# Kernel tuning notes

Hardware: AMD Instinct MI355X
Metric: run time of the kernel (lower is better)

## Reference

```python
import jax, jax.numpy as jnp
import numpy as np

N = 500000
V = 50000
GF = 64
OC = 256

def _lin(key, din, dout):
    k1, k2 = jax.random.split(key)
    w = jax.random.normal(k1, (din, dout), dtype=jnp.float32) * 0.02
    b = jax.random.normal(k2, (dout,), dtype=jnp.float32) * 0.02
    return w, b

def setup_inputs() -> dict:
    key = jax.random.key(0)
    ks = jax.random.split(key, 12)
    inp_feat = jax.random.normal(ks[0], (N, 6), dtype=jnp.float32)
    vox2point_idx = jax.random.randint(ks[1], (N,), 0, V, dtype=jnp.int32)
    w1x, b1x = _lin(ks[2], 3, GF)
    w2x, b2x = _lin(ks[3], GF, OC // 8)
    w1r, b1r = _lin(ks[4], 3, GF)
    w2r, b2r = _lin(ks[5], GF, OC // 8)
    wax, bax = _lin(ks[6], OC // 4, OC // 8)
    war, bar = _lin(ks[7], OC // 4, OC // 8)
    wv1, bv1 = _lin(ks[8], OC // 2, OC // 2)
    w3, b3 = _lin(ks[9], OC, OC)
    w4, b4 = _lin(ks[10], OC, OC)
    wv2, bv2 = _lin(ks[11], OC, OC)
    return dict(inp_feat=inp_feat, vox2point_idx=vox2point_idx, num_vox=V,
                w1x=w1x, b1x=b1x, w2x=w2x, b2x=b2x,
                w1r=w1r, b1r=b1r, w2r=w2r, b2r=b2r,
                wax=wax, bax=bax, war=war, bar=bar,
                wv1=wv1, bv1=bv1, w3=w3, b3=b3, w4=w4, b4=b4,
                wv2=wv2, bv2=bv2)

def reference(inp_feat, vox2point_idx, num_vox,
              w1x, b1x, w2x, b2x, w1r, b1r, w2r, b2r,
              wax, bax, war, bar, wv1, bv1, w3, b3, w4, b4, wv2, bv2):
    relu = jax.nn.relu
    xyz = inp_feat[:, :3]
    rgb = inp_feat[:, 3:]
    fx = relu(relu(xyz @ w1x + b1x) @ w2x + b2x)   # [N, 32]
    fr = relu(relu(rgb @ w1r + b1r) @ w2r + b2r)   # [N, 32]
    comb = jnp.concatenate([fx, fr], axis=-1)       # [N, 64]
    pf2 = jnp.concatenate([
        fx, fx * jax.nn.sigmoid(comb @ wax + bax),
        fr, fr * jax.nn.sigmoid(comb @ war + bar)], axis=-1)  # [N, 128]
    # scatter-max to voxels; torch_scatter fills empty segments with 0 and
    # pf2 >= 0 elementwise, so clamp -inf (jax empty fill) to 0 for parity.
    vox = jax.ops.segment_max(pf2, vox2point_idx, num_segments=num_vox)
    vox = jnp.maximum(vox, 0.0)                     # [V, 128]
    vox = relu(vox @ wv1 + bv1)
    pg = vox[vox2point_idx]                          # gather back [N, 128]
    pf3 = jnp.concatenate([pg, pf2], axis=-1)        # [N, 256]
    pf5 = relu(relu(pf3 @ w3 + b3) @ w4 + b4)        # [N, 256]
    vox2 = jax.ops.segment_max(pf5, vox2point_idx, num_segments=num_vox)
    vox2 = jnp.maximum(vox2, 0.0)
    return relu(vox2 @ wv2 + bv2)                    # [V, 256]
```

## Files before the change

### kernel.cpp

```cpp
#include <hip/hip_runtime.h>

#define NPTS 500000
#define NVOX 50000
#define NBLK 196

typedef unsigned short u16;
typedef unsigned int u32;
typedef __attribute__((ext_vector_type(8))) short short8;
typedef __attribute__((ext_vector_type(4))) float floatx4;
typedef __attribute__((ext_vector_type(4))) unsigned int uintx4;
typedef __attribute__((ext_vector_type(2))) unsigned int uintx2;

__device__ __forceinline__ u16 f2bf(float f) {
    u32 u = __float_as_uint(f);
    u = u + 0x7fffu + ((u >> 16) & 1u);
    return (u16)(u >> 16);
}

__global__ void k_wtransform(const float* __restrict__ W, u16* __restrict__ Wf, int K, int N) {
    int t = blockIdx.x * 256 + threadIdx.x;
    if (t >= K * N) return;
    int k = t / N, n = t - k * N;
    int kk = k >> 5, q = (k >> 3) & 3, j = k & 7;
    Wf[((size_t)((kk * 4 + q) * N + n) << 3) + j] = f2bf(W[t]);
}

__global__ void k_wcat(const float* __restrict__ w2x, const float* __restrict__ w2r, u16* __restrict__ wcatf) {
    int t = blockIdx.x * 256 + threadIdx.x;
    if (t >= 128 * 64) return;
    int k = t >> 6, n = t & 63;
    float v;
    if (k < 64) v = (n < 32) ? w2x[k * 32 + n] : 0.f;
    else        v = (n >= 32) ? w2r[(k - 64) * 32 + (n - 32)] : 0.f;
    int kk = k >> 5, q = (k >> 3) & 3, j = k & 7;
    wcatf[((size_t)((kk * 4 + q) * 64 + n) << 3) + j] = f2bf(v);
}

__global__ void k_watt(const float* __restrict__ wax, const float* __restrict__ war, u16* __restrict__ wattf) {
    int t = blockIdx.x * 256 + threadIdx.x;
    if (t >= 64 * 64) return;
    int k = t >> 6, n = t & 63;
    float v = (n < 32) ? wax[k * 32 + n] : war[k * 32 + (n - 32)];
    int kk = k >> 5, q = (k >> 3) & 3, j = k & 7;
    wattf[((size_t)((kk * 4 + q) * 64 + n) << 3) + j] = f2bf(v);
}

__global__ void k_hist(const int* __restrict__ idx, int* __restrict__ hcnt) {
    int i = blockIdx.x * 256 + threadIdx.x;
    if (i < NPTS) atomicAdd(&hcnt[idx[i]], 1);
}

__global__ __launch_bounds__(256) void k_scan1(const int* __restrict__ hcnt, int* __restrict__ bsum) {
    __shared__ int wsum[4];
    int t = threadIdx.x;
    int i = blockIdx.x * 256 + t;
    int c = (i < NVOX) ? hcnt[i] : 0;
    #pragma unroll
    for (int d = 32; d >= 1; d >>= 1) c += __shfl_xor(c, d, 64);
    if ((t & 63) == 0) wsum[t >> 6] = c;
    __syncthreads();
    if (t == 0) bsum[blockIdx.x] = wsum[0] + wsum[1] + wsum[2] + wsum[3];
}

__global__ __launch_bounds__(256) void k_scan2(const int* __restrict__ bsum, int* __restrict__ boff) {
    __shared__ int wsum[4];
    int t = threadIdx.x, lane = t & 63, w = t >> 6;
    int c = (t < NBLK) ? bsum[t] : 0;
    int v = c;
    #pragma unroll
    for (int d = 1; d < 64; d <<= 1) {
        int o = __shfl_up(v, d, 64);
        if (lane >= d) v += o;
    }
    if (lane == 63) wsum[w] = v;
    __syncthreads();
    int wo = 0;
    #pragma unroll
    for (int k = 0; k < 4; k++) if (k < w) wo += wsum[k];
    if (t < NBLK) boff[t] = wo + v - c;
}

__global__ __launch_bounds__(256) void k_scan3(const int* __restrict__ hcnt, const int* __restrict__ boff,
                                               int* __restrict__ cur) {
    __shared__ int wsum[4];
    int t = threadIdx.x, lane = t & 63, w = t >> 6;
    int i = blockIdx.x * 256 + t;
    int c = (i < NVOX) ? hcnt[i] : 0;
    int v = c;
    #pragma unroll
    for (int d = 1; d < 64; d <<= 1) {
        int o = __shfl_up(v, d, 64);
        if (lane >= d) v += o;
    }
    if (lane == 63) wsum[w] = v;
    __syncthreads();
    int wo = 0;
    #pragma unroll
    for (int k = 0; k < 4; k++) if (k < w) wo += wsum[k];
    if (i < NVOX) cur[i] = boff[blockIdx.x] + wo + v - c;
}

__global__ void k_scatter(const int* __restrict__ idx, int* __restrict__ cur,
                          int* __restrict__ sptid, int* __restrict__ svid) {
    int i = blockIdx.x * 256 + threadIdx.x;
    if (i < NPTS) {
        int v = idx[i];
        int pos = atomicAdd(&cur[v], 1);
        sptid[pos] = i;
        svid[pos] = v;
    }
}

__global__ __launch_bounds__(256) void k_pointfeat(
    const float* __restrict__ inp, const int* __restrict__ sptid, const int* __restrict__ svid,
    const float* __restrict__ w1x, const float* __restrict__ b1x,
    const float* __restrict__ w1r, const float* __restrict__ b1r,
    const u16* __restrict__ wcatf, const float* __restrict__ b2x, const float* __restrict__ b2r,
    const u16* __restrict__ wattf, const float* __restrict__ bax, const float* __restrict__ bar,
    u16* __restrict__ pf2s, float* __restrict__ voxmax)
{
    __shared__ u16 hbuf[64 * 136];
    __shared__ u16 cbuf[64 * 72];
    __shared__ float wl[512];
    __shared__ int lvid[64];
    int t = threadIdx.x;
    int i0 = blockIdx.x * 64;
    int mcnt = NPTS - i0; if (mcnt > 64) mcnt = 64;
    for (int s = t; s < 512; s += 256) {
        float v;
        if (s < 192)      v = w1x[s];
        else if (s < 256) v = b1x[s - 192];
        else if (s < 448) v = w1r[s - 256];
        else              v = b1r[s - 448];
        wl[s] = v;
    }
    if (t < 64) lvid[t] = (t < mcnt) ? svid[i0 + t] : -1;
    __syncthreads();
    {
        int m = t >> 2, c = t & 3;
        float x0 = 0, x1 = 0, x2 = 0, r0 = 0, r1 = 0, r2 = 0;
        if (m < mcnt) {
            const float* p = inp + (size_t)sptid[i0 + m] * 6;
            x0 = p[0]; x1 = p[1]; x2 = p[2]; r0 = p[3]; r1 = p[4]; r2 = p[5];
        }
        u16* hb = &hbuf[m * 136 + c * 16];
        #pragma unroll
        for (int jp = 0; jp < 8; jp++) {
            int c0 = c * 16 + 2 * jp, c1 = c0 + 1;
            float hx0 = fmaxf(wl[192 + c0] + x0 * wl[c0] + x1 * wl[64 + c0] + x2 * wl[128 + c0], 0.f);
            float hx1 = fmaxf(wl[192 + c1] + x0 * wl[c1] + x1 * wl[64 + c1] + x2 * wl[128 + c1], 0.f);
            float hr0 = fmaxf(wl[448 + c0] + r0 * wl[256 + c0] + r1 * wl[320 + c0] + r2 * wl[384 + c0], 0.f);
            float hr1 = fmaxf(wl[448 + c1] + r0 * wl[256 + c1] + r1 * wl[320 + c1] + r2 * wl[384 + c1], 0.f);
            *(u32*)(hb + 2 * jp)      = (u32)f2bf(hx0) | ((u32)f2bf(hx1) << 16);
            *(u32*)(hb + 64 + 2 * jp) = (u32)f2bf(hr0) | ((u32)f2bf(hr1) << 16);
        }
    }
    __syncthreads();
    int wave = t >> 6, l = t & 63, q = l >> 4, lm = l & 15;
    int n = wave * 16 + lm;
    floatx4 acc[4];
    #pragma unroll
    for (int a = 0; a < 4; a++) acc[a] = (floatx4){0.f, 0.f, 0.f, 0.f};
    #pragma unroll
    for (int kk = 0; kk < 4; kk++) {
        short8 bfrag = *(const short8*)&wcatf[(size_t)((kk * 4 + q) * 64 + n) << 3];
        #pragma unroll
        for (int tm = 0; tm < 4; tm++) {
            short8 afrag = *(const short8*)&hbuf[(tm * 16 + lm) * 136 + kk * 32 + q * 8];
            acc[tm] = __builtin_amdgcn_mfma_f32_16x16x32_bf16(afrag, bfrag, acc[tm], 0, 0, 0);
        }
    }
    float bv = (n < 32) ? b2x[n] : b2r[n - 32];
    float comb_keep[4][4];
    #pragma unroll
    for (int tm = 0; tm < 4; tm++)
        #pragma unroll
        for (int r = 0; r < 4; r++) {
            float v = fmaxf(acc[tm][r] + bv, 0.f);
            comb_keep[tm][r] = v;
            int m = tm * 16 + q * 4 + r;
            cbuf[m * 72 + n] = f2bf(v);
        }
    __syncthreads();
    floatx4 acc2[4];
    #pragma unroll
    for (int a = 0; a < 4; a++) acc2[a] = (floatx4){0.f, 0.f, 0.f, 0.f};
    #pragma unroll
    for (int kk = 0; kk < 2; kk++) {
        short8 bfrag = *(const short8*)&wattf[(size_t)((kk * 4 + q) * 64 + n) << 3];
        #pragma unroll
        for (int tm = 0; tm < 4; tm++) {
            short8 afrag = *(const short8*)&cbuf[(tm * 16 + lm) * 72 + kk * 32 + q * 8];
            acc2[tm] = __builtin_amdgcn_mfma_f32_16x16x32_bf16(afrag, bfrag, acc2[tm], 0, 0, 0);
        }
    }
    float bv2 = (n < 32) ? bax[n] : bar[n - 32];
    int pp = (n < 32) ? n : 32 + n;
    #pragma unroll
    for (int tm = 0; tm < 4; tm++)
        #pragma unroll
        for (int r = 0; r < 4; r++) {
            float att = acc2[tm][r] + bv2;
            float sg = 1.f / (1.f + __expf(-att));
            float plain = comb_keep[tm][r];
            float gated = plain * sg;
            int m = tm * 16 + q * 4 + r;
            hbuf[m * 136 + pp] = f2bf(plain);
            hbuf[m * 136 + pp + 32] = f2bf(gated);
        }
    __syncthreads();
    {
        int row = t >> 2, seg = t & 3;
        if (row < mcnt) {
            const u16* src = &hbuf[row * 136 + seg * 32];
            u16* dst = pf2s + (size_t)(i0 + row) * 128 + seg * 32;
            *(uintx4*)dst = *(const uintx4*)src;
            *(uintx4*)(dst + 8) = *(const uintx4*)(src + 8);
        }
    }
    {
        int c2 = t & 63;
        int h = t >> 6;
        int r0 = h * 16;
        int r1 = r0 + 16; if (r1 > mcnt) r1 = mcnt;
        u32 mlo = 0, mhi = 0;
        int pvid = -1;
        for (int r = r0; r < r1; r++) {
            int vid = lvid[r];
            if (vid != pvid) {
                if (pvid >= 0) {
                    int* addr = (int*)(voxmax + (size_t)pvid * 128 + 2 * c2);
                    if (mlo) atomicMax(addr, (int)(mlo << 16));
                    if (mhi) atomicMax(addr + 1, (int)(mhi << 16));
                }
                pvid = vid; mlo = 0; mhi = 0;
            }
            u32 u = *(const u32*)&hbuf[r * 136 + 2 * c2];
            u32 lo = u & 0xffffu, hi = u >> 16;
            mlo = lo > mlo ? lo : mlo;
            mhi = hi > mhi ? hi : mhi;
        }
        if (pvid >= 0) {
            int* addr = (int*)(voxmax + (size_t)pvid * 128 + 2 * c2);
            if (mlo) atomicMax(addr, (int)(mlo << 16));
            if (mhi) atomicMax(addr + 1, (int)(mhi << 16));
        }
    }
}

template<int K, int N, bool ABF16, bool OUT_BF16>
__global__ __launch_bounds__(256) void k_gemm_relu(
    const void* __restrict__ Ap, const u16* __restrict__ Wf,
    const float* __restrict__ bias, void* __restrict__ outp, int M)
{
    constexpr int STRIDE = K + 8;
    constexpr int TN = N / 64;
    constexpr int KSTEPS = K / 32;
    constexpr int CW = K / 4;
    __shared__ u16 lds[64 * STRIDE];
    int i0 = blockIdx.x * 64;
    int mcnt = M - i0; if (mcnt > 64) mcnt = 64;
    int t = threadIdx.x;
    {
        int row = t >> 2, cseg = t & 3;
        u16* dst = &lds[row * STRIDE + cseg * CW];
        if (row < mcnt) {
            if (ABF16) {
                const u16* src = (const u16*)Ap + (size_t)(i0 + row) * K + cseg * CW;
                #pragma unroll
                for (int c = 0; c < CW / 8; c++)
                    *(uintx4*)(dst + c * 8) = *(const uintx4*)(src + c * 8);
            } else {
                const float* src = (const float*)Ap + (size_t)(i0 + row) * K + cseg * CW;
                #pragma unroll
                for (int c = 0; c < CW / 8; c++) {
                    float4 v0 = *(const float4*)(src + c * 8);
                    float4 v1 = *(const float4*)(src + c * 8 + 4);
                    short8 rr;
                    rr[0] = f2bf(v0.x); rr[1] = f2bf(v0.y); rr[2] = f2bf(v0.z); rr[3] = f2bf(v0.w);
                    rr[4] = f2bf(v1.x); rr[5] = f2bf(v1.y); rr[6] = f2bf(v1.z); rr[7] = f2bf(v1.w);
                    *(short8*)(dst + c * 8) = rr;
                }
            }
        } else {
            short8 z = {0, 0, 0, 0, 0, 0, 0, 0};
            #pragma unroll
            for (int c = 0; c < CW / 8; c++) *(short8*)(dst + c * 8) = z;
        }
    }
    __syncthreads();
    int wave = t >> 6, l = t & 63;
    int q = l >> 4, lm = l & 15;
    int wn0 = wave * (N / 4);
    floatx4 acc[4][TN];
    #pragma unroll
    for (int a = 0; a < 4; a++)
        #pragma unroll
        for (int b = 0; b < TN; b++) acc[a][b] = (floatx4){0.f, 0.f, 0.f, 0.f};
    #pragma unroll
    for (int kk = 0; kk < KSTEPS; kk++) {
        short8 afrag[4], bfrag[TN];
        #pragma unroll
        for (int tm = 0; tm < 4; tm++)
            afrag[tm] = *(const short8*)&lds[(tm * 16 + lm) * STRIDE + kk * 32 + q * 8];
        #pragma unroll
        for (int tn = 0; tn < TN; tn++)
            bfrag[tn] = *(const short8*)&Wf[(size_t)((kk * 4 + q) * N + wn0 + tn * 16 + lm) * 8];
        #pragma unroll
        for (int tm = 0; tm < 4; tm++)
            #pragma unroll
            for (int tn = 0; tn < TN; tn++)
                acc[tm][tn] = __builtin_amdgcn_mfma_f32_16x16x32_bf16(afrag[tm], bfrag[tn], acc[tm][tn], 0, 0, 0);
    }
    #pragma unroll
    for (int tm = 0; tm < 4; tm++)
        #pragma unroll
        for (int tn = 0; tn < TN; tn++) {
            int n = wn0 + tn * 16 + lm;
            float bv = bias[n];
            #pragma unroll
            for (int r = 0; r < 4; r++) {
                int m = tm * 16 + q * 4 + r;
                if (m < mcnt) {
                    float v = fmaxf(acc[tm][tn][r] + bv, 0.f);
                    if (OUT_BF16) ((u16*)outp)[(size_t)(i0 + m) * N + n] = f2bf(v);
                    else          ((float*)outp)[(size_t)(i0 + m) * N + n] = v;
                }
            }
        }
}

__global__ __launch_bounds__(256) void k_pointmlp(
    const u16* __restrict__ voxf, const u16* __restrict__ pf2s, const int* __restrict__ svid,
    const u16* __restrict__ w3f, const float* __restrict__ b3,
    const u16* __restrict__ w4f, const float* __restrict__ b4,
    float* __restrict__ vox2)
{
    constexpr int STRIDE = 264;
    __shared__ u16 lds[64 * STRIDE];
    __shared__ int lvid[64];
    __shared__ float bl[512];
    int i0 = blockIdx.x * 64;
    int mcnt = NPTS - i0; if (mcnt > 64) mcnt = 64;
    int t = threadIdx.x;
    if (t < 64) lvid[t] = (t < mcnt) ? svid[i0 + t] : -1;
    for (int s = t; s < 512; s += 256) bl[s] = (s < 256) ? b3[s] : b4[s - 256];
    {
        int row = t >> 2, cseg = t & 3;
        u16* dst = &lds[row * STRIDE + cseg * 64];
        if (row < mcnt) {
            const u16* src;
            if (cseg < 2) src = voxf + (size_t)svid[i0 + row] * 128 + cseg * 64;
            else          src = pf2s + (size_t)(i0 + row) * 128 + (cseg - 2) * 64;
            #pragma unroll
            for (int c = 0; c < 8; c++)
                *(uintx4*)(dst + c * 8) = *(const uintx4*)(src + c * 8);
        } else {
            uintx4 z = {0, 0, 0, 0};
            #pragma unroll
            for (int c = 0; c < 8; c++) *(uintx4*)(dst + c * 8) = z;
        }
    }
    __syncthreads();
    int wave = t >> 6, l = t & 63;
    int q = l >> 4, lm = l & 15;
    int wm0 = wave * 64;
    floatx4 acc[4][4];
    #pragma unroll
    for (int a = 0; a < 4; a++)
        #pragma unroll
        for (int b = 0; b < 4; b++) acc[a][b] = (floatx4){0.f, 0.f, 0.f, 0.f};
    #pragma unroll
    for (int kk = 0; kk < 8; kk++) {
        short8 wfrag[4], bfrag[4];
        #pragma unroll
        for (int tm = 0; tm < 4; tm++)
            wfrag[tm] = *(const short8*)&w3f[(size_t)((kk * 4 + q) * 256 + wm0 + tm * 16 + lm) * 8];
        #pragma unroll
        for (int tn = 0; tn < 4; tn++)
            bfrag[tn] = *(const short8*)&lds[(tn * 16 + lm) * STRIDE + kk * 32 + q * 8];
        #pragma unroll
        for (int tm = 0; tm < 4; tm++)
            #pragma unroll
            for (int tn = 0; tn < 4; tn++)
                acc[tm][tn] = __builtin_amdgcn_mfma_f32_16x16x32_bf16(wfrag[tm], bfrag[tn], acc[tm][tn], 0, 0, 0);
    }
    __syncthreads();
    #pragma unroll
    for (int tm = 0; tm < 4; tm++) {
        float4 bq = *(const float4*)&bl[wm0 + tm * 16 + 4 * q];
        #pragma unroll
        for (int tn = 0; tn < 4; tn++) {
            u32 lo = (u32)f2bf(fmaxf(acc[tm][tn][0] + bq.x, 0.f)) | ((u32)f2bf(fmaxf(acc[tm][tn][1] + bq.y, 0.f)) << 16);
            u32 hi = (u32)f2bf(fmaxf(acc[tm][tn][2] + bq.z, 0.f)) | ((u32)f2bf(fmaxf(acc[tm][tn][3] + bq.w, 0.f)) << 16);
            *(uintx2*)&lds[(tn * 16 + lm) * STRIDE + wm0 + tm * 16 + 4 * q] = (uintx2){lo, hi};
        }
    }
    __syncthreads();
    floatx4 acc2[4][4];
    #pragma unroll
    for (int a = 0; a < 4; a++)
        #pragma unroll
        for (int b = 0; b < 4; b++) acc2[a][b] = (floatx4){0.f, 0.f, 0.f, 0.f};
    #pragma unroll
    for (int kk = 0; kk < 8; kk++) {
        short8 wfrag[4], bfrag[4];
        #pragma unroll
        for (int tm = 0; tm < 4; tm++)
            wfrag[tm] = *(const short8*)&w4f[(size_t)((kk * 4 + q) * 256 + wm0 + tm * 16 + lm) * 8];
        #pragma unroll
        for (int tn = 0; tn < 4; tn++)
            bfrag[tn] = *(const short8*)&lds[(tn * 16 + lm) * STRIDE + kk * 32 + q * 8];
        #pragma unroll
        for (int tm = 0; tm < 4; tm++)
            #pragma unroll
            for (int tn = 0; tn < 4; tn++)
                acc2[tm][tn] = __builtin_amdgcn_mfma_f32_16x16x32_bf16(wfrag[tm], bfrag[tn], acc2[tm][tn], 0, 0, 0);
    }
    __syncthreads();
    #pragma unroll
    for (int tm = 0; tm < 4; tm++) {
        float4 bq = *(const float4*)&bl[256 + wm0 + tm * 16 + 4 * q];
        #pragma unroll
        for (int tn = 0; tn < 4; tn++) {
            u32 lo = (u32)f2bf(fmaxf(acc2[tm][tn][0] + bq.x, 0.f)) | ((u32)f2bf(fmaxf(acc2[tm][tn][1] + bq.y, 0.f)) << 16);
            u32 hi = (u32)f2bf(fmaxf(acc2[tm][tn][2] + bq.z, 0.f)) | ((u32)f2bf(fmaxf(acc2[tm][tn][3] + bq.w, 0.f)) << 16);
            *(uintx2*)&lds[(tn * 16 + lm) * STRIDE + wm0 + tm * 16 + 4 * q] = (uintx2){lo, hi};
        }
    }
    __syncthreads();
    {
        int c2 = t & 127;
        int h = t >> 7;
        int r0 = h * 32;
        int r1 = r0 + 32; if (r1 > mcnt) r1 = mcnt;
        u32 mlo = 0, mhi = 0;
        int pvid = -1;
        for (int r = r0; r < r1; r++) {
            int vid = lvid[r];
            if (vid != pvid) {
                if (pvid >= 0) {
                    int* addr = (int*)(vox2 + (size_t)pvid * 256 + 2 * c2);
                    if (mlo) atomicMax(addr, (int)(mlo << 16));
                    if (mhi) atomicMax(addr + 1, (int)(mhi << 16));
                }
                pvid = vid; mlo = 0; mhi = 0;
            }
            u32 u = *(const u32*)&lds[r * STRIDE + 2 * c2];
            u32 lo = u & 0xffffu, hi = u >> 16;
            mlo = lo > mlo ? lo : mlo;
            mhi = hi > mhi ? hi : mhi;
        }
        if (pvid >= 0) {
            int* addr = (int*)(vox2 + (size_t)pvid * 256 + 2 * c2);
            if (mlo) atomicMax(addr, (int)(mlo << 16));
            if (mhi) atomicMax(addr + 1, (int)(mhi << 16));
        }
    }
}

extern "C" void kernel_launch(void* const* d_in, const int* in_sizes, int n_in,
                              void* d_out, int out_size, void* d_ws, size_t ws_size,
                              hipStream_t stream) {
    const float* inp = (const float*)d_in[0];
    const int*   idx = (const int*)d_in[1];
    const float* w1x = (const float*)d_in[3];  const float* b1x = (const float*)d_in[4];
    const float* w2x = (const float*)d_in[5];  const float* b2x = (const float*)d_in[6];
    const float* w1r = (const float*)d_in[7];  const float* b1r = (const float*)d_in[8];
    const float* w2r = (const float*)d_in[9];  const float* b2r = (const float*)d_in[10];
    const float* wax = (const float*)d_in[11]; const float* bax = (const float*)d_in[12];
    const float* war = (const float*)d_in[13]; const float* bar = (const float*)d_in[14];
    const float* wv1 = (const float*)d_in[15]; const float* bv1 = (const float*)d_in[16];
    const float* w3  = (const float*)d_in[17]; const float* b3  = (const float*)d_in[18];
    const float* w4  = (const float*)d_in[19]; const float* b4  = (const float*)d_in[20];
    const float* wv2 = (const float*)d_in[21]; const float* bv2 = (const float*)d_in[22];
    float* out = (float*)d_out;

    char* ws = (char*)d_ws;
    u16*   pf2s   = (u16*)ws;   ws += (size_t)NPTS * 128 * sizeof(u16);
    float* voxmax = (float*)ws; ws += (size_t)NVOX * 128 * sizeof(float);
    u16*   voxf   = (u16*)ws;   ws += (size_t)NVOX * 128 * sizeof(u16);
    float* vox2   = (float*)ws; ws += (size_t)NVOX * 256 * sizeof(float);
    u16*   w3f    = (u16*)ws;   ws += 65536 * sizeof(u16);
    u16*   w4f    = (u16*)ws;   ws += 65536 * sizeof(u16);
    u16*   wv1f   = (u16*)ws;   ws += 16384 * sizeof(u16);
    u16*   wv2f   = (u16*)ws;   ws += 65536 * sizeof(u16);
    u16*   wcatf  = (u16*)ws;   ws += 8192 * sizeof(u16);
    u16*   wattf  = (u16*)ws;   ws += 4096 * sizeof(u16);
    int*   hcnt   = (int*)ws;   ws += (size_t)NVOX * sizeof(int);
    int*   cur    = (int*)ws;   ws += (size_t)NVOX * sizeof(int);
    int*   bsum   = (int*)ws;   ws += (size_t)NBLK * sizeof(int);
    int*   boff   = (int*)ws;   ws += (size_t)NBLK * sizeof(int);
    int*   sptid  = (int*)ws;   ws += (size_t)NPTS * sizeof(int);
    int*   svid   = (int*)ws;   ws += (size_t)NPTS * sizeof(int);

    hipMemsetAsync(hcnt, 0, (size_t)NVOX * sizeof(int), stream);
    hipMemsetAsync(voxmax, 0, (size_t)NVOX * 128 * sizeof(float), stream);
    hipMemsetAsync(vox2, 0, (size_t)NVOX * 256 * sizeof(float), stream);

    k_wtransform<<<256, 256, 0, stream>>>(w3, w3f, 256, 256);
    k_wtransform<<<256, 256, 0, stream>>>(w4, w4f, 256, 256);
    k_wtransform<<<64,  256, 0, stream>>>(wv1, wv1f, 128, 128);
    k_wtransform<<<256, 256, 0, stream>>>(wv2, wv2f, 256, 256);
    k_wcat<<<32, 256, 0, stream>>>(w2x, w2r, wcatf);
    k_watt<<<16, 256, 0, stream>>>(wax, war, wattf);

    k_hist<<<(NPTS + 255) / 256, 256, 0, stream>>>(idx, hcnt);
    k_scan1<<<NBLK, 256, 0, stream>>>(hcnt, bsum);
    k_scan2<<<1, 256, 0, stream>>>(bsum, boff);
    k_scan3<<<NBLK, 256, 0, stream>>>(hcnt, boff, cur);
    k_scatter<<<(NPTS + 255) / 256, 256, 0, stream>>>(idx, cur, sptid, svid);

    k_pointfeat<<<(NPTS + 63) / 64, 256, 0, stream>>>(
        inp, sptid, svid, w1x, b1x, w1r, b1r, wcatf, b2x, b2r, wattf, bax, bar, pf2s, voxmax);

    k_gemm_relu<128, 128, false, true><<<(NVOX + 63) / 64, 256, 0, stream>>>(
        (const void*)voxmax, wv1f, bv1, (void*)voxf, NVOX);

    k_pointmlp<<<(NPTS + 63) / 64, 256, 0, stream>>>(
        voxf, pf2s, svid, w3f, b3, w4f, b4, vox2);

    k_gemm_relu<256, 256, false, false><<<(NVOX + 63) / 64, 256, 0, stream>>>(
        (const void*)vox2, wv2f, bv2, (void*)out, NVOX);
}
```

Measured before the change: 493.7 us.

## Merge weight prep kernels, widen point kernels to 512 threads, use packed bf16 convert

Fuses the six weight-swizzle launches into one kernel to cut launch overhead. k_pointfeat now handles 128 points per 512-thread block and reuses hbuf in place of the separate cbuf, which needs extra barriers. k_pointmlp splits the same 64-point tile across 8 waves, each holding half the accumulators, to lower register pressure and raise parallelism. Float-to-bf16 packing switches to the hardware packed-convert builtin when it is available, which may round slightly differently.

```diff
diff --git a/kernel.cpp b/kernel.cpp
--- a/kernel.cpp
+++ b/kernel.cpp
@@ -17,32 +17,58 @@
     return (u16)(u >> 16);
 }
 
-__global__ void k_wtransform(const float* __restrict__ W, u16* __restrict__ Wf, int K, int N) {
-    int t = blockIdx.x * 256 + threadIdx.x;
-    if (t >= K * N) return;
+#if defined(__has_builtin)
+#if __has_builtin(__builtin_amdgcn_cvt_pk_bf16_f32)
+#define HAVE_PKBF 1
+#endif
+#endif
+
+__device__ __forceinline__ u32 pkbf(float a, float b) {
+#ifdef HAVE_PKBF
+    typedef __attribute__((ext_vector_type(2))) __bf16 bf16x2;
+    bf16x2 v = __builtin_amdgcn_cvt_pk_bf16_f32(a, b);
+    u32 r; __builtin_memcpy(&r, &v, 4);
+    return r;
+#else
+    return (u32)f2bf(a) | ((u32)f2bf(b) << 16);
+#endif
+}
+
+__device__ __forceinline__ void wswz(const float* __restrict__ W, u16* __restrict__ Wf, int N, int t) {
     int k = t / N, n = t - k * N;
     int kk = k >> 5, q = (k >> 3) & 3, j = k & 7;
     Wf[((size_t)((kk * 4 + q) * N + n) << 3) + j] = f2bf(W[t]);
 }
 
-__global__ void k_wcat(const float* __restrict__ w2x, const float* __restrict__ w2r, u16* __restrict__ wcatf) {
+__global__ __launch_bounds__(256) void k_wprep(
+    const float* __restrict__ w3, const float* __restrict__ w4,
+    const float* __restrict__ wv1, const float* __restrict__ wv2,
+    const float* __restrict__ w2x, const float* __restrict__ w2r,
+    const float* __restrict__ wax, const float* __restrict__ war,
+    u16* __restrict__ w3f, u16* __restrict__ w4f, u16* __restrict__ wv1f, u16* __restrict__ wv2f,
+    u16* __restrict__ wcatf, u16* __restrict__ wattf)
+{
     int t = blockIdx.x * 256 + threadIdx.x;
-    if (t >= 128 * 64) return;
-    int k = t >> 6, n = t & 63;
-    float v;
-    if (k < 64) v = (n < 32) ? w2x[k * 32 + n] : 0.f;
-    else        v = (n >= 32) ? w2r[(k - 64) * 32 + (n - 32)] : 0.f;
-    int kk = k >> 5, q = (k >> 3) & 3, j = k & 7;
-    wcatf[((size_t)((kk * 4 + q) * 64 + n) << 3) + j] = f2bf(v);
-}
-
-__global__ void k_watt(const float* __restrict__ wax, const float* __restrict__ war, u16* __restrict__ wattf) {
-    int t = blockIdx.x * 256 + threadIdx.x;
-    if (t >= 64 * 64) return;
-    int k = t >> 6, n = t & 63;
-    float v = (n < 32) ? wax[k * 32 + n] : war[k * 32 + (n - 32)];
-    int kk = k >> 5, q = (k >> 3) & 3, j = k & 7;
-    wattf[((size_t)((kk * 4 + q) * 64 + n) << 3) + j] = f2bf(v);
+    if (t < 65536) { wswz(w3, w3f, 256, t); return; }  t -= 65536;
+    if (t < 65536) { wswz(w4, w4f, 256, t); return; }  t -= 65536;
+    if (t < 65536) { wswz(wv2, wv2f, 256, t); return; } t -= 65536;
+    if (t < 16384) { wswz(wv1, wv1f, 128, t); return; } t -= 16384;
+    if (t < 8192) {
+        int k = t >> 6, n = t & 63;
+        float v;
+        if (k < 64) v = (n < 32) ? w2x[k * 32 + n] : 0.f;
+        else        v = (n >= 32) ? w2r[(k - 64) * 32 + (n - 32)] : 0.f;
+        int kk = k >> 5, q = (k >> 3) & 3, j = k & 7;
+        wcatf[((size_t)((kk * 4 + q) * 64 + n) << 3) + j] = f2bf(v);
+        return;
+    }
+    t -= 8192;
+    if (t < 4096) {
+        int k = t >> 6, n = t & 63;
+        float v = (n < 32) ? wax[k * 32 + n] : war[k * 32 + (n - 32)];
+        int kk = k >> 5, q = (k >> 3) & 3, j = k & 7;
+        wattf[((size_t)((kk * 4 + q) * 64 + n) << 3) + j] = f2bf(v);
+    }
 }
 
 __global__ void k_hist(const int* __restrict__ idx, int* __restrict__ hcnt) {
@@ -111,7 +137,7 @@
     }
 }
 
-__global__ __launch_bounds__(256) void k_pointfeat(
+__global__ __launch_bounds__(512) void k_pointfeat(
     const float* __restrict__ inp, const int* __restrict__ sptid, const int* __restrict__ svid,
     const float* __restrict__ w1x, const float* __restrict__ b1x,
     const float* __restrict__ w1r, const float* __restrict__ b1r,
@@ -119,22 +145,21 @@
     const u16* __restrict__ wattf, const float* __restrict__ bax, const float* __restrict__ bar,
     u16* __restrict__ pf2s, float* __restrict__ voxmax)
 {
-    __shared__ u16 hbuf[64 * 136];
-    __shared__ u16 cbuf[64 * 72];
+    __shared__ u16 hbuf[128 * 136];
     __shared__ float wl[512];
-    __shared__ int lvid[64];
+    __shared__ int lvid[128];
     int t = threadIdx.x;
-    int i0 = blockIdx.x * 64;
-    int mcnt = NPTS - i0; if (mcnt > 64) mcnt = 64;
-    for (int s = t; s < 512; s += 256) {
+    int i0 = blockIdx.x * 128;
+    int mcnt = NPTS - i0; if (mcnt > 128) mcnt = 128;
+    {
         float v;
-        if (s < 192)      v = w1x[s];
-        else if (s < 256) v = b1x[s - 192];
-        else if (s < 448) v = w1r[s - 256];
-        else              v = b1r[s - 448];
-        wl[s] = v;
-    }
-    if (t < 64) lvid[t] = (t < mcnt) ? svid[i0 + t] : -1;
+        if (t < 192)      v = w1x[t];
+        else if (t < 256) v = b1x[t - 192];
+        else if (t < 448) v = w1r[t - 256];
+        else              v = b1r[t - 448];
+        wl[t] = v;
+    }
+    if (t < 128) lvid[t] = (t < mcnt) ? svid[i0 + t] : -1;
     __syncthreads();
     {
         int m = t >> 2, c = t & 3;
@@ -151,13 +176,14 @@
             float hx1 = fmaxf(wl[192 + c1] + x0 * wl[c1] + x1 * wl[64 + c1] + x2 * wl[128 + c1], 0.f);
             float hr0 = fmaxf(wl[448 + c0] + r0 * wl[256 + c0] + r1 * wl[320 + c0] + r2 * wl[384 + c0], 0.f);
             float hr1 = fmaxf(wl[448 + c1] + r0 * wl[256 + c1] + r1 * wl[320 + c1] + r2 * wl[384 + c1], 0.f);
-            *(u32*)(hb + 2 * jp)      = (u32)f2bf(hx0) | ((u32)f2bf(hx1) << 16);
-            *(u32*)(hb + 64 + 2 * jp) = (u32)f2bf(hr0) | ((u32)f2bf(hr1) << 16);
+            *(u32*)(hb + 2 * jp)      = pkbf(hx0, hx1);
+            *(u32*)(hb + 64 + 2 * jp) = pkbf(hr0, hr1);
         }
     }
     __syncthreads();
     int wave = t >> 6, l = t & 63, q = l >> 4, lm = l & 15;
-    int n = wave * 16 + lm;
+    int n = (wave & 3) * 16 + lm;
+    int rh = (wave >> 2) * 64;
     floatx4 acc[4];
     #pragma unroll
     for (int a = 0; a < 4; a++) acc[a] = (floatx4){0.f, 0.f, 0.f, 0.f};
@@ -166,7 +192,7 @@
         short8 bfrag = *(const short8*)&wcatf[(size_t)((kk * 4 + q) * 64 + n) << 3];
         #pragma unroll
         for (int tm = 0; tm < 4; tm++) {
-            short8 afrag = *(const short8*)&hbuf[(tm * 16 + lm) * 136 + kk * 32 + q * 8];
+            short8 afrag = *(const short8*)&hbuf[(rh + tm * 16 + lm) * 136 + kk * 32 + q * 8];
             acc[tm] = __builtin_amdgcn_mfma_f32_16x16x32_bf16(afrag, bfrag, acc[tm], 0, 0, 0);
         }
     }
@@ -175,11 +201,15 @@
     #pragma unroll
     for (int tm = 0; tm < 4; tm++)
         #pragma unroll
+        for (int r = 0; r < 4; r++)
+            comb_keep[tm][r] = fmaxf(acc[tm][r] + bv, 0.f);
+    __syncthreads();
+    #pragma unroll
+    for (int tm = 0; tm < 4; tm++)
+        #pragma unroll
         for (int r = 0; r < 4; r++) {
-            float v = fmaxf(acc[tm][r] + bv, 0.f);
-            comb_keep[tm][r] = v;
-            int m = tm * 16 + q * 4 + r;
-            cbuf[m * 72 + n] = f2bf(v);
+            int m = rh + tm * 16 + q * 4 + r;
+            hbuf[m * 136 + n] = f2bf(comb_keep[tm][r]);
         }
     __syncthreads();
     floatx4 acc2[4];
@@ -190,10 +220,11 @@
         short8 bfrag = *(const short8*)&wattf[(size_t)((kk * 4 + q) * 64 + n) << 3];
         #pragma unroll
         for (int tm = 0; tm < 4; tm++) {
-            short8 afrag = *(const short8*)&cbuf[(tm * 16 + lm) * 72 + kk * 32 + q * 8];
+            short8 afrag = *(const short8*)&hbuf[(rh + tm * 16 + lm) * 136 + kk * 32 + q * 8];
             acc2[tm] = __builtin_amdgcn_mfma_f32_16x16x32_bf16(afrag, bfrag, acc2[tm], 0, 0, 0);
         }
     }
+    __syncthreads();
     float bv2 = (n < 32) ? bax[n] : bar[n - 32];
     int pp = (n < 32) ? n : 32 + n;
     #pragma unroll
@@ -204,7 +235,7 @@
             float sg = 1.f / (1.f + __expf(-att));
             float plain = comb_keep[tm][r];
             float gated = plain * sg;
-            int m = tm * 16 + q * 4 + r;
+            int m = rh + tm * 16 + q * 4 + r;
             hbuf[m * 136 + pp] = f2bf(plain);
             hbuf[m * 136 + pp + 32] = f2bf(gated);
         }
@@ -276,16 +307,14 @@
                 for (int c = 0; c < CW / 8; c++) {
                     float4 v0 = *(const float4*)(src + c * 8);
                     float4 v1 = *(const float4*)(src + c * 8 + 4);
-                    short8 rr;
-                    rr[0] = f2bf(v0.x); rr[1] = f2bf(v0.y); rr[2] = f2bf(v0.z); rr[3] = f2bf(v0.w);
-                    rr[4] = f2bf(v1.x); rr[5] = f2bf(v1.y); rr[6] = f2bf(v1.z); rr[7] = f2bf(v1.w);
-                    *(short8*)(dst + c * 8) = rr;
+                    uintx4 rr = {pkbf(v0.x, v0.y), pkbf(v0.z, v0.w), pkbf(v1.x, v1.y), pkbf(v1.z, v1.w)};
+                    *(uintx4*)(dst + c * 8) = rr;
                 }
             }
         } else {
-            short8 z = {0, 0, 0, 0, 0, 0, 0, 0};
-            #pragma unroll
-            for (int c = 0; c < CW / 8; c++) *(short8*)(dst + c * 8) = z;
+            uintx4 z = {0, 0, 0, 0};
+            #pragma unroll
+            for (int c = 0; c < CW / 8; c++) *(uintx4*)(dst + c * 8) = z;
         }
     }
     __syncthreads();
@@ -330,7 +359,7 @@
         }
 }
 
-__global__ __launch_bounds__(256) void k_pointmlp(
+__global__ __launch_bounds__(512) void k_pointmlp(
     const u16* __restrict__ voxf, const u16* __restrict__ pf2s, const int* __restrict__ svid,
     const u16* __restrict__ w3f, const float* __restrict__ b3,
     const u16* __restrict__ w4f, const float* __restrict__ b4,
@@ -344,87 +373,87 @@
     int mcnt = NPTS - i0; if (mcnt > 64) mcnt = 64;
     int t = threadIdx.x;
     if (t < 64) lvid[t] = (t < mcnt) ? svid[i0 + t] : -1;
-    for (int s = t; s < 512; s += 256) bl[s] = (s < 256) ? b3[s] : b4[s - 256];
-    {
-        int row = t >> 2, cseg = t & 3;
-        u16* dst = &lds[row * STRIDE + cseg * 64];
+    bl[t] = (t < 256) ? b3[t] : b4[t - 256];
+    {
+        int row = t >> 3, cseg = t & 7;
+        u16* dst = &lds[row * STRIDE + cseg * 32];
         if (row < mcnt) {
             const u16* src;
-            if (cseg < 2) src = voxf + (size_t)svid[i0 + row] * 128 + cseg * 64;
-            else          src = pf2s + (size_t)(i0 + row) * 128 + (cseg - 2) * 64;
-            #pragma unroll
-            for (int c = 0; c < 8; c++)
+            if (cseg < 4) src = voxf + (size_t)svid[i0 + row] * 128 + cseg * 32;
+            else          src = pf2s + (size_t)(i0 + row) * 128 + (cseg - 4) * 32;
+            #pragma unroll
+            for (int c = 0; c < 4; c++)
                 *(uintx4*)(dst + c * 8) = *(const uintx4*)(src + c * 8);
         } else {
             uintx4 z = {0, 0, 0, 0};
             #pragma unroll
-            for (int c = 0; c < 8; c++) *(uintx4*)(dst + c * 8) = z;
+            for (int c = 0; c < 4; c++) *(uintx4*)(dst + c * 8) = z;
         }
     }
     __syncthreads();
     int wave = t >> 6, l = t & 63;
     int q = l >> 4, lm = l & 15;
-    int wm0 = wave * 64;
-    floatx4 acc[4][4];
-    #pragma unroll
-    for (int a = 0; a < 4; a++)
+    int wm0 = wave * 32;
+    floatx4 acc[2][4];
+    #pragma unroll
+    for (int a = 0; a < 2; a++)
         #pragma unroll
         for (int b = 0; b < 4; b++) acc[a][b] = (floatx4){0.f, 0.f, 0.f, 0.f};
     #pragma unroll
     for (int kk = 0; kk < 8; kk++) {
-        short8 wfrag[4], bfrag[4];
-        #pragma unroll
-        for (int tm = 0; tm < 4; tm++)
+        short8 wfrag[2], bfrag[4];
+        #pragma unroll
+        for (int tm = 0; tm < 2; tm++)
             wfrag[tm] = *(const short8*)&w3f[(size_t)((kk * 4 + q) * 256 + wm0 + tm * 16 + lm) * 8];
         #pragma unroll
         for (int tn = 0; tn < 4; tn++)
             bfrag[tn] = *(const short8*)&lds[(tn * 16 + lm) * STRIDE + kk * 32 + q * 8];
         #pragma unroll
-        for (int tm = 0; tm < 4; tm++)
+        for (int tm = 0; tm < 2; tm++)
             #pragma unroll
             for (int tn = 0; tn < 4; tn++)
                 acc[tm][tn] = __builtin_amdgcn_mfma_f32_16x16x32_bf16(wfrag[tm], bfrag[tn], acc[tm][tn], 0, 0, 0);
     }
     __syncthreads();
     #pragma unroll
-    for (int tm = 0; tm < 4; tm++) {
+    for (int tm = 0; tm < 2; tm++) {
         float4 bq = *(const float4*)&bl[wm0 + tm * 16 + 4 * q];
         #pragma unroll
         for (int tn = 0; tn < 4; tn++) {
-            u32 lo = (u32)f2bf(fmaxf(acc[tm][tn][0] + bq.x, 0.f)) | ((u32)f2bf(fmaxf(acc[tm][tn][1] + bq.y, 0.f)) << 16);
-            u32 hi = (u32)f2bf(fmaxf(acc[tm][tn][2] + bq.z, 0.f)) | ((u32)f2bf(fmaxf(acc[tm][tn][3] + bq.w, 0.f)) << 16);
+            u32 lo = pkbf(fmaxf(acc[tm][tn][0] + bq.x, 0.f), fmaxf(acc[tm][tn][1] + bq.y, 0.f));
+            u32 hi = pkbf(fmaxf(acc[tm][tn][2] + bq.z, 0.f), fmaxf(acc[tm][tn][3] + bq.w, 0.f));
             *(uintx2*)&lds[(tn * 16 + lm) * STRIDE + wm0 + tm * 16 + 4 * q] = (uintx2){lo, hi};
         }
     }
     __syncthreads();
-    floatx4 acc2[4][4];
-    #pragma unroll
-    for (int a = 0; a < 4; a++)
+    floatx4 acc2[2][4];
+    #pragma unroll
+    for (int a = 0; a < 2; a++)
         #pragma unroll
         for (int b = 0; b < 4; b++) acc2[a][b] = (floatx4){0.f, 0.f, 0.f, 0.f};
     #pragma unroll
     for (int kk = 0; kk < 8; kk++) {
-        short8 wfrag[4], bfrag[4];
-        #pragma unroll
-        for (int tm = 0; tm < 4; tm++)
+        short8 wfrag[2], bfrag[4];
+        #pragma unroll
+        for (int tm = 0; tm < 2; tm++)
             wfrag[tm] = *(const short8*)&w4f[(size_t)((kk * 4 + q) * 256 + wm0 + tm * 16 + lm) * 8];
         #pragma unroll
         for (int tn = 0; tn < 4; tn++)
             bfrag[tn] = *(const short8*)&lds[(tn * 16 + lm) * STRIDE + kk * 32 + q * 8];
         #pragma unroll
-        for (int tm = 0; tm < 4; tm++)
+        for (int tm = 0; tm < 2; tm++)
             #pragma unroll
             for (int tn = 0; tn < 4; tn++)
                 acc2[tm][tn] = __builtin_amdgcn_mfma_f32_16x16x32_bf16(wfrag[tm], bfrag[tn], acc2[tm][tn], 0, 0, 0);
     }
     __syncthreads();
     #pragma unroll
-    for (int tm = 0; tm < 4; tm++) {
+    for (int tm = 0; tm < 2; tm++) {
         float4 bq = *(const float4*)&bl[256 + wm0 + tm * 16 + 4 * q];
         #pragma unroll
         for (int tn = 0; tn < 4; tn++) {
-            u32 lo = (u32)f2bf(fmaxf(acc2[tm][tn][0] + bq.x, 0.f)) | ((u32)f2bf(fmaxf(acc2[tm][tn][1] + bq.y, 0.f)) << 16);
-            u32 hi = (u32)f2bf(fmaxf(acc2[tm][tn][2] + bq.z, 0.f)) | ((u32)f2bf(fmaxf(acc2[tm][tn][3] + bq.w, 0.f)) << 16);
+            u32 lo = pkbf(fmaxf(acc2[tm][tn][0] + bq.x, 0.f), fmaxf(acc2[tm][tn][1] + bq.y, 0.f));
+            u32 hi = pkbf(fmaxf(acc2[tm][tn][2] + bq.z, 0.f), fmaxf(acc2[tm][tn][3] + bq.w, 0.f));
             *(uintx2*)&lds[(tn * 16 + lm) * STRIDE + wm0 + tm * 16 + 4 * q] = (uintx2){lo, hi};
         }
     }
@@ -432,8 +461,8 @@
     {
         int c2 = t & 127;
         int h = t >> 7;
-        int r0 = h * 32;
-        int r1 = r0 + 32; if (r1 > mcnt) r1 = mcnt;
+        int r0 = h * 16;
+        int r1 = r0 + 16; if (r1 > mcnt) r1 = mcnt;
         u32 mlo = 0, mhi = 0;
         int pvid = -1;
         for (int r = r0; r < r1; r++) {
@@ -498,12 +527,8 @@
     hipMemsetAsync(voxmax, 0, (size_t)NVOX * 128 * sizeof(float), stream);
     hipMemsetAsync(vox2, 0, (size_t)NVOX * 256 * sizeof(float), stream);
 
-    k_wtransform<<<256, 256, 0, stream>>>(w3, w3f, 256, 256);
-    k_wtransform<<<256, 256, 0, stream>>>(w4, w4f, 256, 256);
-    k_wtransform<<<64,  256, 0, stream>>>(wv1, wv1f, 128, 128);
-    k_wtransform<<<256, 256, 0, stream>>>(wv2, wv2f, 256, 256);
-    k_wcat<<<32, 256, 0, stream>>>(w2x, w2r, wcatf);
-    k_watt<<<16, 256, 0, stream>>>(wax, war, wattf);
+    k_wprep<<<880, 256, 0, stream>>>(w3, w4, wv1, wv2, w2x, w2r, wax, war,
+                                     w3f, w4f, wv1f, wv2f, wcatf, wattf);
 
     k_hist<<<(NPTS + 255) / 256, 256, 0, stream>>>(idx, hcnt);
     k_scan1<<<NBLK, 256, 0, stream>>>(hcnt, bsum);
@@ -511,13 +536,13 @@
     k_scan3<<<NBLK, 256, 0, stream>>>(hcnt, boff, cur);
     k_scatter<<<(NPTS + 255) / 256, 256, 0, stream>>>(idx, cur, sptid, svid);
 
-    k_pointfeat<<<(NPTS + 63) / 64, 256, 0, stream>>>(
+    k_pointfeat<<<(NPTS + 127) / 128, 512, 0, stream>>>(
         inp, sptid, svid, w1x, b1x, w1r, b1r, wcatf, b2x, b2r, wattf, bax, bar, pf2s, voxmax);
 
     k_gemm_relu<128, 128, false, true><<<(NVOX + 63) / 64, 256, 0, stream>>>(
         (const void*)voxmax, wv1f, bv1, (void*)voxf, NVOX);
 
-    k_pointmlp<<<(NPTS + 63) / 64, 256, 0, stream>>>(
+    k_pointmlp<<<(NPTS + 63) / 64, 512, 0, stream>>>(
         voxf, pf2s, svid, w3f, b3, w4f, b4, vox2);
 
     k_gemm_relu<256, 256, false, false><<<(NVOX + 63) / 64, 256, 0, stream>>>(
```

Measured after the change: 514.9 us. 1.04x slower.

## Fuse weight prep kernels, MFMA first layer, packed bf16 converts, wider scatter-max

Applied to the files above, without the earlier changes.

Merges the six weight-transform launches into one k_wprep kernel and adds a swizzled bf16 first-layer weight with the biases folded in through a constant-one input column. The first 3->64 layers for xyz and rgb now run as one MFMA over a padded 32-wide K in place of scalar FMAs from shared memory. Float-to-bf16 packing uses the hardware packed-convert builtin when it is available. The scatter-max loops fold the shift into the load and handle four channels per thread in the second kernel. The aim is fewer launches and less ALU work, at the cost of bf16 rounding of the raw inputs in the first layer, which adds precision error.

```diff
diff --git a/kernel.cpp b/kernel.cpp
--- a/kernel.cpp
+++ b/kernel.cpp
@@ -17,32 +17,75 @@
     return (u16)(u >> 16);
 }
 
-__global__ void k_wtransform(const float* __restrict__ W, u16* __restrict__ Wf, int K, int N) {
-    int t = blockIdx.x * 256 + threadIdx.x;
-    if (t >= K * N) return;
+#if defined(__has_builtin)
+#if __has_builtin(__builtin_amdgcn_cvt_pk_bf16_f32)
+#define HAVE_PKBF 1
+#endif
+#endif
+
+__device__ __forceinline__ u32 pkbf(float a, float b) {
+#ifdef HAVE_PKBF
+    typedef __attribute__((ext_vector_type(2))) __bf16 bf16x2;
+    bf16x2 v = __builtin_amdgcn_cvt_pk_bf16_f32(a, b);
+    u32 r; __builtin_memcpy(&r, &v, 4);
+    return r;
+#else
+    return (u32)f2bf(a) | ((u32)f2bf(b) << 16);
+#endif
+}
+
+__device__ __forceinline__ void wswz(const float* __restrict__ W, u16* __restrict__ Wf, int N, int t) {
     int k = t / N, n = t - k * N;
     int kk = k >> 5, q = (k >> 3) & 3, j = k & 7;
     Wf[((size_t)((kk * 4 + q) * N + n) << 3) + j] = f2bf(W[t]);
 }
 
-__global__ void k_wcat(const float* __restrict__ w2x, const float* __restrict__ w2r, u16* __restrict__ wcatf) {
+__global__ __launch_bounds__(256) void k_wprep(
+    const float* __restrict__ w3, const float* __restrict__ w4,
+    const float* __restrict__ wv1, const float* __restrict__ wv2,
+    const float* __restrict__ w2x, const float* __restrict__ w2r,
+    const float* __restrict__ wax, const float* __restrict__ war,
+    const float* __restrict__ w1x, const float* __restrict__ b1x,
+    const float* __restrict__ w1r, const float* __restrict__ b1r,
+    u16* __restrict__ w3f, u16* __restrict__ w4f, u16* __restrict__ wv1f, u16* __restrict__ wv2f,
+    u16* __restrict__ wcatf, u16* __restrict__ wattf, u16* __restrict__ w1ef)
+{
     int t = blockIdx.x * 256 + threadIdx.x;
-    if (t >= 128 * 64) return;
-    int k = t >> 6, n = t & 63;
-    float v;
-    if (k < 64) v = (n < 32) ? w2x[k * 32 + n] : 0.f;
-    else        v = (n >= 32) ? w2r[(k - 64) * 32 + (n - 32)] : 0.f;
-    int kk = k >> 5, q = (k >> 3) & 3, j = k & 7;
-    wcatf[((size_t)((kk * 4 + q) * 64 + n) << 3) + j] = f2bf(v);
-}
-
-__global__ void k_watt(const float* __restrict__ wax, const float* __restrict__ war, u16* __restrict__ wattf) {
-    int t = blockIdx.x * 256 + threadIdx.x;
-    if (t >= 64 * 64) return;
-    int k = t >> 6, n = t & 63;
-    float v = (n < 32) ? wax[k * 32 + n] : war[k * 32 + (n - 32)];
-    int kk = k >> 5, q = (k >> 3) & 3, j = k & 7;
-    wattf[((size_t)((kk * 4 + q) * 64 + n) << 3) + j] = f2bf(v);
+    if (t < 65536) { wswz(w3, w3f, 256, t); return; }  t -= 65536;
+    if (t < 65536) { wswz(w4, w4f, 256, t); return; }  t -= 65536;
+    if (t < 65536) { wswz(wv2, wv2f, 256, t); return; } t -= 65536;
+    if (t < 16384) { wswz(wv1, wv1f, 128, t); return; } t -= 16384;
+    if (t < 8192) {
+        int k = t >> 6, n = t & 63;
+        float v;
+        if (k < 64) v = (n < 32) ? w2x[k * 32 + n] : 0.f;
+        else        v = (n >= 32) ? w2r[(k - 64) * 32 + (n - 32)] : 0.f;
+        int kk = k >> 5, q = (k >> 3) & 3, j = k & 7;
+        wcatf[((size_t)((kk * 4 + q) * 64 + n) << 3) + j] = f2bf(v);
+        return;
+    }
+    t -= 8192;
+    if (t < 4096) {
+        int k = t >> 6, n = t & 63;
+        float v = (n < 32) ? wax[k * 32 + n] : war[k * 32 + (n - 32)];
+        int kk = k >> 5, q = (k >> 3) & 3, j = k & 7;
+        wattf[((size_t)((kk * 4 + q) * 64 + n) << 3) + j] = f2bf(v);
+        return;
+    }
+    t -= 4096;
+    if (t < 4096) {
+        int k = t >> 7, n = t & 127;
+        float v = 0.f;
+        if (n < 64) {
+            if (k < 3)       v = w1x[k * 64 + n];
+            else if (k == 3) v = b1x[n];
+        } else {
+            if (k >= 4 && k < 7) v = w1r[(k - 4) * 64 + (n - 64)];
+            else if (k == 7)     v = b1r[n - 64];
+        }
+        int q = (k >> 3) & 3, j = k & 7;
+        w1ef[((size_t)(q * 128 + n) << 3) + j] = f2bf(v);
+    }
 }
 
 __global__ void k_hist(const int* __restrict__ idx, int* __restrict__ hcnt) {
@@ -113,50 +156,69 @@
 
 __global__ __launch_bounds__(256) void k_pointfeat(
     const float* __restrict__ inp, const int* __restrict__ sptid, const int* __restrict__ svid,
-    const float* __restrict__ w1x, const float* __restrict__ b1x,
-    const float* __restrict__ w1r, const float* __restrict__ b1r,
+    const u16* __restrict__ w1ef,
     const u16* __restrict__ wcatf, const float* __restrict__ b2x, const float* __restrict__ b2r,
     const u16* __restrict__ wattf, const float* __restrict__ bax, const float* __restrict__ bar,
     u16* __restrict__ pf2s, float* __restrict__ voxmax)
 {
     __shared__ u16 hbuf[64 * 136];
     __shared__ u16 cbuf[64 * 72];
-    __shared__ float wl[512];
+    __shared__ u16 abuf[64 * 40];
     __shared__ int lvid[64];
     int t = threadIdx.x;
     int i0 = blockIdx.x * 64;
     int mcnt = NPTS - i0; if (mcnt > 64) mcnt = 64;
-    for (int s = t; s < 512; s += 256) {
-        float v;
-        if (s < 192)      v = w1x[s];
-        else if (s < 256) v = b1x[s - 192];
-        else if (s < 448) v = w1r[s - 256];
-        else              v = b1r[s - 448];
-        wl[s] = v;
-    }
     if (t < 64) lvid[t] = (t < mcnt) ? svid[i0 + t] : -1;
-    __syncthreads();
     {
         int m = t >> 2, c = t & 3;
-        float x0 = 0, x1 = 0, x2 = 0, r0 = 0, r1 = 0, r2 = 0;
-        if (m < mcnt) {
-            const float* p = inp + (size_t)sptid[i0 + m] * 6;
-            x0 = p[0]; x1 = p[1]; x2 = p[2]; r0 = p[3]; r1 = p[4]; r2 = p[5];
-        }
-        u16* hb = &hbuf[m * 136 + c * 16];
-        #pragma unroll
-        for (int jp = 0; jp < 8; jp++) {
-            int c0 = c * 16 + 2 * jp, c1 = c0 + 1;
-            float hx0 = fmaxf(wl[192 + c0] + x0 * wl[c0] + x1 * wl[64 + c0] + x2 * wl[128 + c0], 0.f);
-            float hx1 = fmaxf(wl[192 + c1] + x0 * wl[c1] + x1 * wl[64 + c1] + x2 * wl[128 + c1], 0.f);
-            float hr0 = fmaxf(wl[448 + c0] + r0 * wl[256 + c0] + r1 * wl[320 + c0] + r2 * wl[384 + c0], 0.f);
-            float hr1 = fmaxf(wl[448 + c1] + r0 * wl[256 + c1] + r1 * wl[320 + c1] + r2 * wl[384 + c1], 0.f);
-            *(u32*)(hb + 2 * jp)      = (u32)f2bf(hx0) | ((u32)f2bf(hx1) << 16);
-            *(u32*)(hb + 64 + 2 * jp) = (u32)f2bf(hr0) | ((u32)f2bf(hr1) << 16);
-        }
+        u16* ab = &abuf[m * 40];
+        bool act = (m < mcnt);
+        if (c < 3) {
+            float2 v = {0.f, 0.f};
+            if (act) v = *(const float2*)(inp + (size_t)sptid[i0 + m] * 6 + 2 * c);
+            if (c == 0)      { ab[0] = f2bf(v.x); ab[1] = f2bf(v.y); }
+            else if (c == 1) { ab[2] = f2bf(v.x); ab[4] = f2bf(v.y); }
+            else             { ab[5] = f2bf(v.x); ab[6] = f2bf(v.y); }
+        } else {
+            u16 one = act ? (u16)0x3F80 : (u16)0;
+            ab[3] = one; ab[7] = one;
+        }
+        #pragma unroll
+        for (int z = 0; z < 3; z++) *(u32*)&ab[8 + 6 * c + 2 * z] = 0;
     }
     __syncthreads();
     int wave = t >> 6, l = t & 63, q = l >> 4, lm = l & 15;
+    {
+        floatx4 hacc[4][2];
+        #pragma unroll
+        for (int a = 0; a < 4; a++)
+            #pragma unroll
+            for (int b = 0; b < 2; b++) hacc[a][b] = (floatx4){0.f, 0.f, 0.f, 0.f};
+        short8 bfrag[2], afrag[4];
+        #pragma unroll
+        for (int tn = 0; tn < 2; tn++)
+            bfrag[tn] = *(const short8*)&w1ef[(size_t)(q * 128 + wave * 32 + tn * 16 + lm) * 8];
+        #pragma unroll
+        for (int tm = 0; tm < 4; tm++)
+            afrag[tm] = *(const short8*)&abuf[(tm * 16 + lm) * 40 + q * 8];
+        #pragma unroll
+        for (int tm = 0; tm < 4; tm++)
+            #pragma unroll
+            for (int tn = 0; tn < 2; tn++)
+                hacc[tm][tn] = __builtin_amdgcn_mfma_f32_16x16x32_bf16(afrag[tm], bfrag[tn], hacc[tm][tn], 0, 0, 0);
+        #pragma unroll
+        for (int tm = 0; tm < 4; tm++)
+            #pragma unroll
+            for (int tn = 0; tn < 2; tn++) {
+                int n2 = wave * 32 + tn * 16 + lm;
+                #pragma unroll
+                for (int r = 0; r < 4; r++) {
+                    int m = tm * 16 + q * 4 + r;
+                    hbuf[m * 136 + n2] = f2bf(fmaxf(hacc[tm][tn][r], 0.f));
+                }
+            }
+    }
+    __syncthreads();
     int n = wave * 16 + lm;
     floatx4 acc[4];
     #pragma unroll
@@ -230,20 +292,20 @@
             if (vid != pvid) {
                 if (pvid >= 0) {
                     int* addr = (int*)(voxmax + (size_t)pvid * 128 + 2 * c2);
-                    if (mlo) atomicMax(addr, (int)(mlo << 16));
-                    if (mhi) atomicMax(addr + 1, (int)(mhi << 16));
+                    if (mlo) atomicMax(addr, (int)mlo);
+                    if (mhi) atomicMax(addr + 1, (int)mhi);
                 }
                 pvid = vid; mlo = 0; mhi = 0;
             }
             u32 u = *(const u32*)&hbuf[r * 136 + 2 * c2];
-            u32 lo = u & 0xffffu, hi = u >> 16;
+            u32 lo = u << 16, hi = u & 0xffff0000u;
             mlo = lo > mlo ? lo : mlo;
             mhi = hi > mhi ? hi : mhi;
         }
         if (pvid >= 0) {
             int* addr = (int*)(voxmax + (size_t)pvid * 128 + 2 * c2);
-            if (mlo) atomicMax(addr, (int)(mlo << 16));
-            if (mhi) atomicMax(addr + 1, (int)(mhi << 16));
+            if (mlo) atomicMax(addr, (int)mlo);
+            if (mhi) atomicMax(addr + 1, (int)mhi);
         }
     }
 }
@@ -276,16 +338,14 @@
                 for (int c = 0; c < CW / 8; c++) {
                     float4 v0 = *(const float4*)(src + c * 8);
                     float4 v1 = *(const float4*)(src + c * 8 + 4);
-                    short8 rr;
-                    rr[0] = f2bf(v0.x); rr[1] = f2bf(v0.y); rr[2] = f2bf(v0.z); rr[3] = f2bf(v0.w);
-                    rr[4] = f2bf(v1.x); rr[5] = f2bf(v1.y); rr[6] = f2bf(v1.z); rr[7] = f2bf(v1.w);
-                    *(short8*)(dst + c * 8) = rr;
+                    uintx4 rr = {pkbf(v0.x, v0.y), pkbf(v0.z, v0.w), pkbf(v1.x, v1.y), pkbf(v1.z, v1.w)};
+                    *(uintx4*)(dst + c * 8) = rr;
                 }
             }
         } else {
-            short8 z = {0, 0, 0, 0, 0, 0, 0, 0};
-            #pragma unroll
-            for (int c = 0; c < CW / 8; c++) *(short8*)(dst + c * 8) = z;
+            uintx4 z = {0, 0, 0, 0};
+            #pragma unroll
+            for (int c = 0; c < CW / 8; c++) *(uintx4*)(dst + c * 8) = z;
         }
     }
     __syncthreads();
@@ -391,8 +451,8 @@
         float4 bq = *(const float4*)&bl[wm0 + tm * 16 + 4 * q];
         #pragma unroll
         for (int tn = 0; tn < 4; tn++) {
-            u32 lo = (u32)f2bf(fmaxf(acc[tm][tn][0] + bq.x, 0.f)) | ((u32)f2bf(fmaxf(acc[tm][tn][1] + bq.y, 0.f)) << 16);
-            u32 hi = (u32)f2bf(fmaxf(acc[tm][tn][2] + bq.z, 0.f)) | ((u32)f2bf(fmaxf(acc[tm][tn][3] + bq.w, 0.f)) << 16);
+            u32 lo = pkbf(fmaxf(acc[tm][tn][0] + bq.x, 0.f), fmaxf(acc[tm][tn][1] + bq.y, 0.f));
+            u32 hi = pkbf(fmaxf(acc[tm][tn][2] + bq.z, 0.f), fmaxf(acc[tm][tn][3] + bq.w, 0.f));
             *(uintx2*)&lds[(tn * 16 + lm) * STRIDE + wm0 + tm * 16 + 4 * q] = (uintx2){lo, hi};
         }
     }
@@ -423,38 +483,45 @@
         float4 bq = *(const float4*)&bl[256 + wm0 + tm * 16 + 4 * q];
         #pragma unroll
         for (int tn = 0; tn < 4; tn++) {
-            u32 lo = (u32)f2bf(fmaxf(acc2[tm][tn][0] + bq.x, 0.f)) | ((u32)f2bf(fmaxf(acc2[tm][tn][1] + bq.y, 0.f)) << 16);
-            u32 hi = (u32)f2bf(fmaxf(acc2[tm][tn][2] + bq.z, 0.f)) | ((u32)f2bf(fmaxf(acc2[tm][tn][3] + bq.w, 0.f)) << 16);
+            u32 lo = pkbf(fmaxf(acc2[tm][tn][0] + bq.x, 0.f), fmaxf(acc2[tm][tn][1] + bq.y, 0.f));
+            u32 hi = pkbf(fmaxf(acc2[tm][tn][2] + bq.z, 0.f), fmaxf(acc2[tm][tn][3] + bq.w, 0.f));
             *(uintx2*)&lds[(tn * 16 + lm) * STRIDE + wm0 + tm * 16 + 4 * q] = (uintx2){lo, hi};
         }
     }
     __syncthreads();
     {
-        int c2 = t & 127;
-        int h = t >> 7;
-        int r0 = h * 32;
-        int r1 = r0 + 32; if (r1 > mcnt) r1 = mcnt;
-        u32 mlo = 0, mhi = 0;
+        int c4 = t & 63;
+        int g = t >> 6;
+        int r0 = g * 16;
+        int r1 = r0 + 16; if (r1 > mcnt) r1 = mcnt;
+        u32 m0 = 0, m1 = 0, m2 = 0, m3 = 0;
         int pvid = -1;
         for (int r = r0; r < r1; r++) {
             int vid = lvid[r];
             if (vid != pvid) {
                 if (pvid >= 0) {
-                    int* addr = (int*)(vox2 + (size_t)pvid * 256 + 2 * c2);
-                    if (mlo) atomicMax(addr, (int)(mlo << 16));
-                    if (mhi) atomicMax(addr + 1, (int)(mhi << 16));
+                    int* addr = (int*)(vox2 + (size_t)pvid * 256 + 4 * c4);
+                    if (m0) atomicMax(addr,     (int)m0);
+                    if (m1) atomicMax(addr + 1, (int)m1);
+                    if (m2) atomicMax(addr + 2, (int)m2);
+                    if (m3) atomicMax(addr + 3, (int)m3);
                 }
-                pvid = vid; mlo = 0; mhi = 0;
+                pvid = vid; m0 = m1 = m2 = m3 = 0;
             }
-            u32 u = *(const u32*)&lds[r * STRIDE + 2 * c2];
-            u32 lo = u & 0xffffu, hi = u >> 16;
-            mlo = lo > mlo ? lo : mlo;
-            mhi = hi > mhi ? hi : mhi;
+            uintx2 u = *(const uintx2*)&lds[r * STRIDE + 4 * c4];
+            u32 a0 = u[0] << 16, a1 = u[0] & 0xffff0000u;
+            u32 a2 = u[1] << 16, a3 = u[1] & 0xffff0000u;
+            m0 = a0 > m0 ? a0 : m0;
+            m1 = a1 > m1 ? a1 : m1;
+            m2 = a2 > m2 ? a2 : m2;
+            m3 = a3 > m3 ? a3 : m3;
         }
         if (pvid >= 0) {
-            int* addr = (int*)(vox2 + (size_t)pvid * 256 + 2 * c2);
-            if (mlo) atomicMax(addr, (int)(mlo << 16));
-            if (mhi) atomicMax(addr + 1, (int)(mhi << 16));
+            int* addr = (int*)(vox2 + (size_t)pvid * 256 + 4 * c4);
+            if (m0) atomicMax(addr,     (int)m0);
+            if (m1) atomicMax(addr + 1, (int)m1);
+            if (m2) atomicMax(addr + 2, (int)m2);
+            if (m3) atomicMax(addr + 3, (int)m3);
         }
     }
 }
@@ -487,6 +554,7 @@
     u16*   wv2f   = (u16*)ws;   ws += 65536 * sizeof(u16);
     u16*   wcatf  = (u16*)ws;   ws += 8192 * sizeof(u16);
     u16*   wattf  = (u16*)ws;   ws += 4096 * sizeof(u16);
+    u16*   w1ef   = (u16*)ws;   ws += 4096 * sizeof(u16);
     int*   hcnt   = (int*)ws;   ws += (size_t)NVOX * sizeof(int);
     int*   cur    = (int*)ws;   ws += (size_t)NVOX * sizeof(int);
     int*   bsum   = (int*)ws;   ws += (size_t)NBLK * sizeof(int);
@@ -498,12 +566,9 @@
     hipMemsetAsync(voxmax, 0, (size_t)NVOX * 128 * sizeof(float), stream);
     hipMemsetAsync(vox2, 0, (size_t)NVOX * 256 * sizeof(float), stream);
 
-    k_wtransform<<<256, 256, 0, stream>>>(w3, w3f, 256, 256);
-    k_wtransform<<<256, 256, 0, stream>>>(w4, w4f, 256, 256);
-    k_wtransform<<<64,  256, 0, stream>>>(wv1, wv1f, 128, 128);
-    k_wtransform<<<256, 256, 0, stream>>>(wv2, wv2f, 256, 256);
-    k_wcat<<<32, 256, 0, stream>>>(w2x, w2r, wcatf);
-    k_watt<<<16, 256, 0, stream>>>(wax, war, wattf);
+    k_wprep<<<896, 256, 0, stream>>>(w3, w4, wv1, wv2, w2x, w2r, wax, war,
+                                     w1x, b1x, w1r, b1r,
+                                     w3f, w4f, wv1f, wv2f, wcatf, wattf, w1ef);
 
     k_hist<<<(NPTS + 255) / 256, 256, 0, stream>>>(idx, hcnt);
     k_scan1<<<NBLK, 256, 0, stream>>>(hcnt, bsum);
@@ -512,7 +577,7 @@
     k_scatter<<<(NPTS + 255) / 256, 256, 0, stream>>>(idx, cur, sptid, svid);
 
     k_pointfeat<<<(NPTS + 63) / 64, 256, 0, stream>>>(
-        inp, sptid, svid, w1x, b1x, w1r, b1r, wcatf, b2x, b2r, wattf, bax, bar, pf2s, voxmax);
+        inp, sptid, svid, w1ef, wcatf, b2x, b2r, wattf, bax, bar, pf2s, voxmax);
 
     k_gemm_relu<128, 128, false, true><<<(NVOX + 63) / 64, 256, 0, stream>>>(
         (const void*)voxmax, wv1f, bv1, (void*)voxf, NVOX);
```

Result: slower. 545.9 us (+10.6%).
